# Performance work log

Measured on AMD Instinct MI355X. Metric: run time of the kernel, lower is better.

The kernel has to match this reference:

```python
import jax, jax.numpy as jnp
import numpy as np

N_NODES = 50000
N_EDGES = 600000
D = 128
N_GRAPHS = 500


def setup_inputs() -> dict:
    key = jax.random.key(0)
    ks = jax.random.split(key, 8)
    node_feats = jax.random.normal(ks[0], (N_NODES, D), dtype=jnp.float32)
    W1 = jax.random.normal(ks[1], (D, D), dtype=jnp.float32) * (1.0 / np.sqrt(D))
    b1 = jnp.zeros((D,), dtype=jnp.float32)
    W2 = jax.random.normal(ks[2], (D, D), dtype=jnp.float32) * (1.0 / np.sqrt(D))
    b2 = jnp.zeros((D,), dtype=jnp.float32)
    src = jax.random.randint(ks[3], (N_EDGES,), 0, N_NODES, dtype=jnp.int32)
    dst = jax.random.randint(ks[4], (N_EDGES,), 0, N_NODES, dtype=jnp.int32)
    graph_ids = jnp.sort(jax.random.randint(ks[5], (N_NODES,), 0, N_GRAPHS, dtype=jnp.int32))
    return {"node_feats": node_feats, "W1": W1, "b1": b1, "W2": W2, "b2": b2,
            "src": src, "dst": dst, "graph_ids": graph_ids}


def _graph_conv(h, W, b, src, dst, norm_src, norm_dst, n_nodes):
    # DGL GraphConv, norm='both': D_in^{-1/2} A D_out^{-1/2} X W + b
    hs = h * norm_src[:, None]                     # (N, D) scale by out-degree^-1/2
    m = jax.ops.segment_sum(hs[src], dst, num_segments=n_nodes)  # sparse aggregate
    return (m * norm_dst[:, None]) @ W + b


def reference(node_feats, W1, b1, W2, b2, src, dst, graph_ids):
    n = node_feats.shape[0]
    ones_e = jnp.ones(src.shape, dtype=node_feats.dtype)
    deg_out = jnp.maximum(jax.ops.segment_sum(ones_e, src, num_segments=n), 1.0)
    deg_in = jnp.maximum(jax.ops.segment_sum(ones_e, dst, num_segments=n), 1.0)
    norm_src = deg_out ** -0.5
    norm_dst = deg_in ** -0.5
    # NOTE: original code builds num_layers-1 = 2 GraphConv layers for num_layers=3
    h = jax.nn.relu(_graph_conv(node_feats, W1, b1, src, dst, norm_src, norm_dst, n))
    h = jax.nn.relu(_graph_conv(h, W2, b2, src, dst, norm_src, norm_dst, n))
    # AvgPooling: per-graph mean of node features
    sums = jax.ops.segment_sum(h, graph_ids, num_segments=N_GRAPHS)
    counts = jnp.maximum(
        jax.ops.segment_sum(jnp.ones((n,), h.dtype), graph_ids, num_segments=N_GRAPHS), 1.0)
    return sums / counts[:, None]
```

## Files before the change

kernel.cpp:

```cpp
#include <hip/hip_runtime.h>

#define D 128

typedef __attribute__((ext_vector_type(8))) short bf16x8;
typedef __attribute__((ext_vector_type(4))) float f32x4;

__device__ __forceinline__ unsigned int f32_to_bf16_rne(float x) {
    unsigned int u = __float_as_uint(x);
    return (u + 0x7FFFu + ((u >> 16) & 1u)) >> 16;
}
__device__ __forceinline__ float bf16_val(float x) {
    return __uint_as_float(f32_to_bf16_rne(x) << 16);
}

__global__ void scatter_count_wprep_kernel(
    const int* __restrict__ src, const int* __restrict__ dst,
    int* __restrict__ cnt_out, int* __restrict__ deg_in,
    unsigned short* __restrict__ bucket, int E, int S, int eblocks,
    const float* __restrict__ W1, const float* __restrict__ W2,
    unsigned short* __restrict__ wt) {
    if ((int)blockIdx.x < eblocks) {
        int e = blockIdx.x * 256 + threadIdx.x;
        if (e < E) {
            int s = src[e];
            int d = dst[e];
            int pos = atomicAdd(&deg_in[d], 1);
            if (pos < S) bucket[(size_t)d * S + pos] = (unsigned short)s;
            atomicAdd(&cnt_out[s], 1);
        }
    } else {
        int i = (blockIdx.x - eblocks) * 256 + threadIdx.x;
        if (i < 2 * 16384) {
            int w = i >> 14, idx = i & 16383;
            int k = idx >> 7, col = idx & 127;
            float v = (w == 0 ? W1 : W2)[idx];
            unsigned int hi = f32_to_bf16_rne(v);
            float lo = v - __uint_as_float(hi << 16);
            int kc = k >> 5, quad = (k >> 3) & 3, j = k & 7;
            size_t slot = (size_t)kc * 4096 + quad * 1024 + col * 8 + j;
            wt[(size_t)w * 32768 + slot] = (unsigned short)hi;
            wt[(size_t)w * 32768 + 16384 + slot] = (unsigned short)f32_to_bf16_rne(lo);
        }
    }
}

__global__ void prep_kernel(const int* __restrict__ cnt_out, const int* __restrict__ cnt_in,
                            float* __restrict__ norm_src, float* __restrict__ norm_dst,
                            const float2* __restrict__ x, unsigned int* __restrict__ xb,
                            int N, int n2, int nbA) {
    int b = blockIdx.x;
    if (b < nbA) {
        int i = b * 256 + threadIdx.x;
        if (i < N) {
            norm_src[i] = 1.0f / sqrtf(fmaxf((float)cnt_out[i], 1.0f));
            norm_dst[i] = 1.0f / sqrtf(fmaxf((float)cnt_in[i], 1.0f));
        }
    } else {
        int i = (b - nbA) * 256 + threadIdx.x;
        if (i < n2) {
            int row = i >> 6;
            float s = 1.0f / sqrtf(fmaxf((float)cnt_out[row], 1.0f));
            float2 v = x[i];
            xb[i] = f32_to_bf16_rne(v.x * s) | (f32_to_bf16_rne(v.y * s) << 16);
        }
    }
}

#define AGG_STEP(J) do {                                                       \
        int sj = ss[J];                                                        \
        uint2 uj = featb2[(size_t)sj * 32 + c];                                \
        acc.x += __uint_as_float(uj.x << 16);                                  \
        acc.y += __uint_as_float(uj.x & 0xFFFF0000u);                          \
        acc.z += __uint_as_float(uj.y << 16);                                  \
        acc.w += __uint_as_float(uj.y & 0xFFFF0000u);                          \
    } while (0)

template <bool OUT_BF16>
__global__ __launch_bounds__(512, 8) void agg_mfma_kernel(
    const uint2* __restrict__ featb2, const float* __restrict__ norm_src,
    const float* __restrict__ norm_dst, const int* __restrict__ deg_in,
    const unsigned short* __restrict__ bucket,
    const unsigned short* __restrict__ wthi, const unsigned short* __restrict__ wtlo,
    const float* __restrict__ bias, void* __restrict__ outp, int N, int S) {
    __shared__ unsigned int mtp[2][16][68];
    int node0 = blockIdx.x * 16;
    int ng = threadIdx.x >> 5;
    int c  = threadIdx.x & 31;
    int node = node0 + ng;

    float4 acc = make_float4(0.f, 0.f, 0.f, 0.f);
    if (node < N) {
        int len = min(deg_in[node], S);
        const unsigned short* row = bucket + (size_t)node * S;
        int e = 0;
        for (; e + 8 <= len; e += 8) {
            ushort4 sa = *(const ushort4*)(row + e);
            ushort4 sb = *(const ushort4*)(row + e + 4);
            int ss[8] = {sa.x, sa.y, sa.z, sa.w, sb.x, sb.y, sb.z, sb.w};
            AGG_STEP(0); AGG_STEP(1); AGG_STEP(2); AGG_STEP(3);
            AGG_STEP(4); AGG_STEP(5); AGG_STEP(6); AGG_STEP(7);
        }
        for (; e + 4 <= len; e += 4) {
            ushort4 sa = *(const ushort4*)(row + e);
            int ss[4] = {sa.x, sa.y, sa.z, sa.w};
            AGG_STEP(0); AGG_STEP(1); AGG_STEP(2); AGG_STEP(3);
        }
        for (; e < len; e++) {
            int ss[1] = {row[e]};
            AGG_STEP(0);
        }
    }
    float hx = bf16_val(acc.x), hy = bf16_val(acc.y);
    float hz = bf16_val(acc.z), hw = bf16_val(acc.w);
    mtp[0][ng][2 * c]     = f32_to_bf16_rne(acc.x) | (f32_to_bf16_rne(acc.y) << 16);
    mtp[0][ng][2 * c + 1] = f32_to_bf16_rne(acc.z) | (f32_to_bf16_rne(acc.w) << 16);
    mtp[1][ng][2 * c]     = f32_to_bf16_rne(acc.x - hx) | (f32_to_bf16_rne(acc.y - hy) << 16);
    mtp[1][ng][2 * c + 1] = f32_to_bf16_rne(acc.z - hz) | (f32_to_bf16_rne(acc.w - hw) << 16);
    __syncthreads();

    int lane = threadIdx.x & 63;
    int wv   = threadIdx.x >> 6;
    int n16  = lane & 15;
    int quad = lane >> 4;
    int col  = wv * 16 + n16;
    f32x4 dacc = {0.f, 0.f, 0.f, 0.f};
#pragma unroll
    for (int kc = 0; kc < 4; kc++) {
        int ko = kc * 32 + quad * 8;
        int bo = kc * 4096 + quad * 1024 + col * 8;
        bf16x8 ahi = *(const bf16x8*)((const unsigned short*)mtp[0][n16] + ko);
        bf16x8 alo = *(const bf16x8*)((const unsigned short*)mtp[1][n16] + ko);
        bf16x8 bhi = *(const bf16x8*)(wthi + bo);
        bf16x8 blo = *(const bf16x8*)(wtlo + bo);
        dacc = __builtin_amdgcn_mfma_f32_16x16x32_bf16(ahi, bhi, dacc, 0, 0, 0);
        dacc = __builtin_amdgcn_mfma_f32_16x16x32_bf16(ahi, blo, dacc, 0, 0, 0);
        dacc = __builtin_amdgcn_mfma_f32_16x16x32_bf16(alo, bhi, dacc, 0, 0, 0);
    }
    float bv = bias[col];
#pragma unroll
    for (int r = 0; r < 4; r++) {
        int n = node0 + quad * 4 + r;
        if (n < N) {
            float v = fmaxf(fmaf(dacc[r], norm_dst[n], bv), 0.f);
            if (OUT_BF16) {
                ((unsigned short*)outp)[(size_t)n * D + col] =
                    (unsigned short)f32_to_bf16_rne(v * norm_src[n]);
            } else {
                ((float*)outp)[(size_t)n * D + col] = v;
            }
        }
    }
}

__global__ void pool_kernel(const float* __restrict__ h, const int* __restrict__ gids,
                            float* __restrict__ out, int N, int G) {
    __shared__ float part[128];
    int g = blockIdx.x;
    int f = threadIdx.x & 127;
    int half = threadIdx.x >> 7;
    int lo = 0, hi = N;
    while (lo < hi) { int mid = (lo + hi) >> 1; if (gids[mid] < g) lo = mid + 1; else hi = mid; }
    int start = lo;
    hi = N;
    while (lo < hi) { int mid = (lo + hi) >> 1; if (gids[mid] < g + 1) lo = mid + 1; else hi = mid; }
    int end = lo;

    float s0 = 0.f, s1 = 0.f, s2 = 0.f, s3 = 0.f;
    int n = start + half;
    for (; n + 6 < end; n += 8) {
        s0 += h[(size_t)(n + 0) * D + f];
        s1 += h[(size_t)(n + 2) * D + f];
        s2 += h[(size_t)(n + 4) * D + f];
        s3 += h[(size_t)(n + 6) * D + f];
    }
    for (; n < end; n += 2) s0 += h[(size_t)n * D + f];
    float s = (s0 + s1) + (s2 + s3);
    if (half == 1) part[f] = s;
    __syncthreads();
    if (half == 0) {
        float cnt = (float)(end - start);
        out[(size_t)g * D + f] = (s + part[f]) / fmaxf(cnt, 1.0f);
    }
}

extern "C" void kernel_launch(void* const* d_in, const int* in_sizes, int n_in,
                              void* d_out, int out_size, void* d_ws, size_t ws_size,
                              hipStream_t stream) {
    const float* node_feats = (const float*)d_in[0];
    const float* W1 = (const float*)d_in[1];
    const float* b1 = (const float*)d_in[2];
    const float* W2 = (const float*)d_in[3];
    const float* b2 = (const float*)d_in[4];
    const int*   src = (const int*)d_in[5];
    const int*   dst = (const int*)d_in[6];
    const int*   gid = (const int*)d_in[7];

    int N = in_sizes[7];
    int E = in_sizes[5];
    int G = out_size / D;

    size_t npad = ((size_t)N + 255) & ~(size_t)255;

    int S = 64;
    while (S > 32) {
        size_t need = (4 * npad + npad * (size_t)(S / 2)
                       + (size_t)N * D / 2 * 2
                       + (size_t)N * D
                       + 32768) * sizeof(float);
        if (need <= ws_size) break;
        S -= 16;
    }

    float* ws       = (float*)d_ws;
    float* norm_src = ws;
    float* norm_dst = ws + npad;
    int*   cnt_out  = (int*)(ws + 2 * npad);
    int*   deg_in   = (int*)(ws + 3 * npad);
    unsigned short* bucket = (unsigned short*)(ws + 4 * npad);
    unsigned int* xb  = (unsigned int*)(ws + 4 * npad + npad * (size_t)(S / 2));
    unsigned int* h1b = xb + (size_t)N * D / 2;
    float* h2       = (float*)(h1b + (size_t)N * D / 2);
    unsigned short* wt = (unsigned short*)(h2 + (size_t)N * D);
    float* out      = (float*)d_out;

    (void)hipMemsetAsync(cnt_out, 0, 2 * npad * sizeof(int), stream);
    int eblocks = (E + 255) / 256;
    int wblocks = (2 * 16384 + 255) / 256;
    scatter_count_wprep_kernel<<<eblocks + wblocks, 256, 0, stream>>>(
        src, dst, cnt_out, deg_in, bucket, E, S, eblocks, W1, W2, wt);
    int n2 = N * (D / 2);
    int nbA = (N + 255) / 256;
    int nbB = (n2 + 255) / 256;
    prep_kernel<<<nbA + nbB, 256, 0, stream>>>(cnt_out, deg_in, norm_src, norm_dst,
                                               (const float2*)node_feats, xb, N, n2, nbA);

    int blocks = (N + 15) / 16;

    agg_mfma_kernel<true><<<blocks, 512, 0, stream>>>(
        (const uint2*)xb, norm_src, norm_dst, deg_in, bucket,
        wt, wt + 16384, b1, h1b, N, S);
    agg_mfma_kernel<false><<<blocks, 512, 0, stream>>>(
        (const uint2*)h1b, norm_src, norm_dst, deg_in, bucket,
        wt + 32768, wt + 49152, b2, h2, N, S);

    pool_kernel<<<G, 256, 0, stream>>>(h2, gid, out, N, G);
}
```

Baseline: 223.6 us.

## Fold prep kernel into scatter and compute degree norms on the fly

Removes the separate prep kernel. The bf16 conversion of the input features now runs as extra blocks in the scatter/weight-prep launch, without the source-degree scaling. Layer-1 aggregation instead applies the per-source rsqrt norm to each gathered neighbour from cnt_out, and the epilogue recomputes the dst and src norms from the degree counts. This saves a launch and the norm arrays, at the cost of an extra random gather of cnt_out and an rsqrt per edge in layer 1.

```diff
diff --git a/kernel.cpp b/kernel.cpp
--- a/kernel.cpp
+++ b/kernel.cpp
@@ -13,14 +13,16 @@
     return __uint_as_float(f32_to_bf16_rne(x) << 16);
 }
 
-__global__ void scatter_count_wprep_kernel(
+__global__ void scatter_count_wprep_cvt_kernel(
     const int* __restrict__ src, const int* __restrict__ dst,
     int* __restrict__ cnt_out, int* __restrict__ deg_in,
-    unsigned short* __restrict__ bucket, int E, int S, int eblocks,
+    unsigned short* __restrict__ bucket, int E, int S, int eblocks, int wblocks,
     const float* __restrict__ W1, const float* __restrict__ W2,
-    unsigned short* __restrict__ wt) {
-    if ((int)blockIdx.x < eblocks) {
-        int e = blockIdx.x * 256 + threadIdx.x;
+    unsigned short* __restrict__ wt,
+    const float2* __restrict__ x, unsigned int* __restrict__ xb, int n2) {
+    int b = blockIdx.x;
+    if (b < eblocks) {
+        int e = b * 256 + threadIdx.x;
         if (e < E) {
             int s = src[e];
             int d = dst[e];
@@ -28,8 +30,8 @@
             if (pos < S) bucket[(size_t)d * S + pos] = (unsigned short)s;
             atomicAdd(&cnt_out[s], 1);
         }
-    } else {
-        int i = (blockIdx.x - eblocks) * 256 + threadIdx.x;
+    } else if (b < eblocks + wblocks) {
+        int i = (b - eblocks) * 256 + threadIdx.x;
         if (i < 2 * 16384) {
             int w = i >> 14, idx = i & 16383;
             int k = idx >> 7, col = idx & 127;
@@ -41,27 +43,11 @@
             wt[(size_t)w * 32768 + slot] = (unsigned short)hi;
             wt[(size_t)w * 32768 + 16384 + slot] = (unsigned short)f32_to_bf16_rne(lo);
         }
-    }
-}
-
-__global__ void prep_kernel(const int* __restrict__ cnt_out, const int* __restrict__ cnt_in,
-                            float* __restrict__ norm_src, float* __restrict__ norm_dst,
-                            const float2* __restrict__ x, unsigned int* __restrict__ xb,
-                            int N, int n2, int nbA) {
-    int b = blockIdx.x;
-    if (b < nbA) {
-        int i = b * 256 + threadIdx.x;
-        if (i < N) {
-            norm_src[i] = 1.0f / sqrtf(fmaxf((float)cnt_out[i], 1.0f));
-            norm_dst[i] = 1.0f / sqrtf(fmaxf((float)cnt_in[i], 1.0f));
-        }
     } else {
-        int i = (b - nbA) * 256 + threadIdx.x;
+        int i = (b - eblocks - wblocks) * 256 + threadIdx.x;
         if (i < n2) {
-            int row = i >> 6;
-            float s = 1.0f / sqrtf(fmaxf((float)cnt_out[row], 1.0f));
             float2 v = x[i];
-            xb[i] = f32_to_bf16_rne(v.x * s) | (f32_to_bf16_rne(v.y * s) << 16);
+            xb[i] = f32_to_bf16_rne(v.x) | (f32_to_bf16_rne(v.y) << 16);
         }
     }
 }
@@ -69,17 +55,24 @@
 #define AGG_STEP(J) do {                                                       \
         int sj = ss[J];                                                        \
         uint2 uj = featb2[(size_t)sj * 32 + c];                                \
-        acc.x += __uint_as_float(uj.x << 16);                                  \
-        acc.y += __uint_as_float(uj.x & 0xFFFF0000u);                          \
-        acc.z += __uint_as_float(uj.y << 16);                                  \
-        acc.w += __uint_as_float(uj.y & 0xFFFF0000u);                          \
+        if (SCALE_SRC) {                                                       \
+            float nj = 1.0f / sqrtf(fmaxf((float)cnt_out[sj], 1.0f));          \
+            acc.x = fmaf(__uint_as_float(uj.x << 16), nj, acc.x);              \
+            acc.y = fmaf(__uint_as_float(uj.x & 0xFFFF0000u), nj, acc.y);      \
+            acc.z = fmaf(__uint_as_float(uj.y << 16), nj, acc.z);              \
+            acc.w = fmaf(__uint_as_float(uj.y & 0xFFFF0000u), nj, acc.w);      \
+        } else {                                                               \
+            acc.x += __uint_as_float(uj.x << 16);                              \
+            acc.y += __uint_as_float(uj.x & 0xFFFF0000u);                      \
+            acc.z += __uint_as_float(uj.y << 16);                              \
+            acc.w += __uint_as_float(uj.y & 0xFFFF0000u);                      \
+        }                                                                      \
     } while (0)
 
-template <bool OUT_BF16>
+template <bool SCALE_SRC, bool OUT_BF16>
 __global__ __launch_bounds__(512, 8) void agg_mfma_kernel(
-    const uint2* __restrict__ featb2, const float* __restrict__ norm_src,
-    const float* __restrict__ norm_dst, const int* __restrict__ deg_in,
-    const unsigned short* __restrict__ bucket,
+    const uint2* __restrict__ featb2, const int* __restrict__ cnt_out,
+    const int* __restrict__ deg_in, const unsigned short* __restrict__ bucket,
     const unsigned short* __restrict__ wthi, const unsigned short* __restrict__ wtlo,
     const float* __restrict__ bias, void* __restrict__ outp, int N, int S) {
     __shared__ unsigned int mtp[2][16][68];
@@ -141,10 +134,12 @@
     for (int r = 0; r < 4; r++) {
         int n = node0 + quad * 4 + r;
         if (n < N) {
-            float v = fmaxf(fmaf(dacc[r], norm_dst[n], bv), 0.f);
+            float nd = 1.0f / sqrtf(fmaxf((float)deg_in[n], 1.0f));
+            float v = fmaxf(fmaf(dacc[r], nd, bv), 0.f);
             if (OUT_BF16) {
+                float ns = 1.0f / sqrtf(fmaxf((float)cnt_out[n], 1.0f));
                 ((unsigned short*)outp)[(size_t)n * D + col] =
-                    (unsigned short)f32_to_bf16_rne(v * norm_src[n]);
+                    (unsigned short)f32_to_bf16_rne(v * ns);
             } else {
                 ((float*)outp)[(size_t)n * D + col] = v;
             }
@@ -203,7 +198,7 @@
 
     int S = 64;
     while (S > 32) {
-        size_t need = (4 * npad + npad * (size_t)(S / 2)
+        size_t need = (2 * npad + npad * (size_t)(S / 2)
                        + (size_t)N * D / 2 * 2
                        + (size_t)N * D
                        + 32768) * sizeof(float);
@@ -212,35 +207,31 @@
     }
 
     float* ws       = (float*)d_ws;
-    float* norm_src = ws;
-    float* norm_dst = ws + npad;
-    int*   cnt_out  = (int*)(ws + 2 * npad);
-    int*   deg_in   = (int*)(ws + 3 * npad);
-    unsigned short* bucket = (unsigned short*)(ws + 4 * npad);
-    unsigned int* xb  = (unsigned int*)(ws + 4 * npad + npad * (size_t)(S / 2));
+    int*   cnt_out  = (int*)ws;
+    int*   deg_in   = (int*)(ws + npad);
+    unsigned short* bucket = (unsigned short*)(ws + 2 * npad);
+    unsigned int* xb  = (unsigned int*)(ws + 2 * npad + npad * (size_t)(S / 2));
     unsigned int* h1b = xb + (size_t)N * D / 2;
     float* h2       = (float*)(h1b + (size_t)N * D / 2);
     unsigned short* wt = (unsigned short*)(h2 + (size_t)N * D);
     float* out      = (float*)d_out;
 
     (void)hipMemsetAsync(cnt_out, 0, 2 * npad * sizeof(int), stream);
+    int n2 = N * (D / 2);
     int eblocks = (E + 255) / 256;
     int wblocks = (2 * 16384 + 255) / 256;
-    scatter_count_wprep_kernel<<<eblocks + wblocks, 256, 0, stream>>>(
-        src, dst, cnt_out, deg_in, bucket, E, S, eblocks, W1, W2, wt);
-    int n2 = N * (D / 2);
-    int nbA = (N + 255) / 256;
-    int nbB = (n2 + 255) / 256;
-    prep_kernel<<<nbA + nbB, 256, 0, stream>>>(cnt_out, deg_in, norm_src, norm_dst,
-                                               (const float2*)node_feats, xb, N, n2, nbA);
+    int cblocks = (n2 + 255) / 256;
+    scatter_count_wprep_cvt_kernel<<<eblocks + wblocks + cblocks, 256, 0, stream>>>(
+        src, dst, cnt_out, deg_in, bucket, E, S, eblocks, wblocks,
+        W1, W2, wt, (const float2*)node_feats, xb, n2);
 
     int blocks = (N + 15) / 16;
 
-    agg_mfma_kernel<true><<<blocks, 512, 0, stream>>>(
-        (const uint2*)xb, norm_src, norm_dst, deg_in, bucket,
+    agg_mfma_kernel<true, true><<<blocks, 512, 0, stream>>>(
+        (const uint2*)xb, cnt_out, deg_in, bucket,
         wt, wt + 16384, b1, h1b, N, S);
-    agg_mfma_kernel<false><<<blocks, 512, 0, stream>>>(
-        (const uint2*)h1b, norm_src, norm_dst, deg_in, bucket,
+    agg_mfma_kernel<false, false><<<blocks, 512, 0, stream>>>(
+        (const uint2*)h1b, cnt_out, deg_in, bucket,
         wt + 32768, wt + 49152, b2, h2, N, S);
 
     pool_kernel<<<G, 256, 0, stream>>>(h2, gid, out, N, G);
```

New measurement: 241.3 us. +7.9%, slower.
